# Kernel tuning notes

Measured on AMD Instinct MI355X. Metric: run time of the kernel, lower is better.

## Reference

```python
import jax, jax.numpy as jnp
import numpy as np

B, NF, H = 1024, 64, 512


def setup_inputs() -> dict:
    key = jax.random.key(0)
    ks = jax.random.split(key, 12)
    sc_in2 = 1.0 / np.sqrt(2 * H)
    sc_in1 = 1.0 / np.sqrt(H)
    inp = {
        "field_vectors": jax.random.normal(ks[0], (B, NF, H), dtype=jnp.float32),
        # and_fusion: Linear(2H->H), ReLU, Linear(H->H)
        "and_W1": jax.random.uniform(ks[1], (2 * H, H), jnp.float32, -sc_in2, sc_in2),
        "and_b1": jax.random.uniform(ks[2], (H,), jnp.float32, -sc_in2, sc_in2),
        "and_W2": jax.random.uniform(ks[3], (H, H), jnp.float32, -sc_in1, sc_in1),
        "and_b2": jax.random.uniform(ks[4], (H,), jnp.float32, -sc_in1, sc_in1),
        # or_fusion: Linear(2H->H), ReLU, Linear(H->H)
        "or_W1": jax.random.uniform(ks[5], (2 * H, H), jnp.float32, -sc_in2, sc_in2),
        "or_b1": jax.random.uniform(ks[6], (H,), jnp.float32, -sc_in2, sc_in2),
        "or_W2": jax.random.uniform(ks[7], (H, H), jnp.float32, -sc_in1, sc_in1),
        "or_b2": jax.random.uniform(ks[8], (H,), jnp.float32, -sc_in1, sc_in1),
        # not_transform: Linear(H->H), Tanh
        "not_W": jax.random.uniform(ks[9], (H, H), jnp.float32, -sc_in1, sc_in1),
        "not_b": jax.random.uniform(ks[10], (H,), jnp.float32, -sc_in1, sc_in1),
        # Disjoint index structure so the torch skip-set logic is a no-op:
        # 'and' pairs use fields 0..31, 'or' pairs use 32..47, leftovers 48..63.
        "not_idx": 48 + jnp.arange(8, dtype=jnp.int32),
        "and_pairs": jnp.arange(32, dtype=jnp.int32).reshape(16, 2),
        "or_pairs": (32 + jnp.arange(16, dtype=jnp.int32)).reshape(8, 2),
        "leftover_idx": 48 + jnp.arange(16, dtype=jnp.int32),
    }
    return inp


def _mlp2(x, W1, b1, W2, b2):
    # Linear -> ReLU -> Linear
    return jax.nn.relu(x @ W1 + b1) @ W2 + b2


def reference(field_vectors, and_W1, and_b1, and_W2, and_b2,
              or_W1, or_b1, or_W2, or_b2, not_W, not_b,
              not_idx, and_pairs, or_pairs, leftover_idx):
    # In-place 'not' transform on selected fields (Tanh(Linear))
    fv = field_vectors.at[:, not_idx].set(
        jnp.tanh(field_vectors[:, not_idx] @ not_W + not_b))
    # Gather (i, j) pairs, concat along feature dim -> [B, P, 2H]
    cat_and = jnp.concatenate([fv[:, and_pairs[:, 0]], fv[:, and_pairs[:, 1]]], axis=-1)
    fused_and = _mlp2(cat_and, and_W1, and_b1, and_W2, and_b2)  # [B, 16, H]
    cat_or = jnp.concatenate([fv[:, or_pairs[:, 0]], fv[:, or_pairs[:, 1]]], axis=-1)
    fused_or = _mlp2(cat_or, or_W1, or_b1, or_W2, or_b2)  # [B, 8, H]
    # Stack order matches torch loop: and results, or results, untouched fields
    return jnp.concatenate([fused_and, fused_or, fv[:, leftover_idx]], axis=1)
```

## Files before the change

### kernel.cpp

```cpp
#include <hip/hip_runtime.h>
#include <hip/hip_bf16.h>
#include <math.h>

typedef __attribute__((ext_vector_type(8))) __bf16 bf16x8;
typedef __attribute__((ext_vector_type(4))) float f32x4;

__device__ __forceinline__ unsigned short f2bf(float f) {
    union { float f; unsigned u; } v; v.f = f;
    unsigned r = v.u + 0x7fffu + ((v.u >> 16) & 1u);
    return (unsigned short)(r >> 16);
}
__device__ __forceinline__ unsigned int pk(float a, float b) {
    union { float f; unsigned u; } x, y; x.f = a; y.f = b;
    unsigned ra = (x.u + 0x7fffu + ((x.u >> 16) & 1u)) >> 16;
    unsigned rb = (y.u + 0x7fffu + ((y.u >> 16) & 1u)) & 0xffff0000u;
    return ra | rb;
}

__device__ __forceinline__ void gl2lds16(const unsigned short* g, unsigned short* l) {
    __builtin_amdgcn_global_load_lds(
        (const __attribute__((address_space(1))) unsigned int*)(g),
        (__attribute__((address_space(3))) unsigned int*)(l), 16, 0, 0);
}

struct SetupArgs {
    const int *and_pairs, *or_pairs, *not_idx, *lidx;
    int* tbl;
    const float* W[5];
    unsigned short* WT[5];
    int K[5], N[5];
    int tstart[6];
};

__global__ __launch_bounds__(256) void setup_kernel(SetupArgs a) {
    __shared__ float tile[64][65];
    const int blk = blockIdx.x;
    const int tid = threadIdx.x;

    if (blk == 0) {
        if (tid < 64) {
            const int f = tid;
            int u = 0;
            for (int i = 0; i < 32; i++) u |= (a.and_pairs[i] == f);
            for (int i = 0; i < 16; i++) u |= (a.or_pairs[i] == f);
            int isnot = 0;
            for (int i = 0; i < 8; i++)  isnot |= (a.not_idx[i] == f);
            int ls = -1;
            for (int l = 0; l < 16; l++) if (a.lidx[l] == f) ls = l;
            if (isnot) ls = -1;
            a.tbl[f] = (u | isnot) | ((ls + 1) << 8);
        }
        return;
    }

    const int bx = blk - 1;
    int m = 0;
    while (bx >= a.tstart[m + 1]) m++;
    const float* src = a.W[m];
    unsigned short* dst = a.WT[m];
    const int K = a.K[m], N = a.N[m];
    const int t = bx - a.tstart[m];
    const int ntn = N >> 6;
    const int tk = t / ntn, tn = t % ntn;
    const int c = tid & 63, r0 = tid >> 6;
    #pragma unroll
    for (int r = r0; r < 64; r += 4)
        tile[r][c] = src[(size_t)(tk * 64 + r) * N + tn * 64 + c];
    __syncthreads();
    const int l = tid & 63;
    #pragma unroll
    for (int fi = tid >> 6; fi < 8; fi += 4) {
        const int ktl = fi & 1, cgl = fi >> 1;
        const int kt = tk * 2 + ktl, cg = tn * 4 + cgl;
        const int kb = ktl * 32 + (l >> 4) * 8;
        const int nb = cgl * 16 + (l & 15);
        uint4 o;
        o.x = pk(tile[kb + 0][nb], tile[kb + 1][nb]);
        o.y = pk(tile[kb + 2][nb], tile[kb + 3][nb]);
        o.z = pk(tile[kb + 4][nb], tile[kb + 5][nb]);
        o.w = pk(tile[kb + 6][nb], tile[kb + 7][nb]);
        ((uint4*)dst)[((size_t)kt * 32 + cg) * 64 + l] = o;
    }
}

struct PrepArgs {
    const float* fv;
    unsigned short* fvb;
    const int* tbl;
    float* out;
};

__global__ __launch_bounds__(256) void prep_kernel(PrepArgs a) {
    const int t = blockIdx.x * 256 + threadIdx.x;
    const size_t e = (size_t)t * 8;
    const int c = (int)(e & 511);
    const int f = (int)((e >> 9) & 63);
    const int b = (int)(e >> 15);
    const float4 v0 = *(const float4*)(a.fv + e);
    const float4 v1 = *(const float4*)(a.fv + e + 4);
    const int tb = a.tbl[f];
    const int u  = tb & 0xff;
    const int ls = (tb >> 8) - 1;
    if (u) {
        uint4 o;
        o.x = pk(v0.x, v0.y); o.y = pk(v0.z, v0.w);
        o.z = pk(v1.x, v1.y); o.w = pk(v1.z, v1.w);
        ((uint4*)a.fvb)[t] = o;
    }
    if (ls >= 0) {
        float* d = a.out + ((size_t)b * 40 + 24 + ls) * 512 + c;
        *(float4*)(d)     = v0;
        *(float4*)(d + 4) = v1;
    }
}

#define LOADB(DST, WTP, KD, K0)                                              \
    _Pragma("unroll") for (int ni = 0; ni < 8; ni++)                         \
        DST[ni] = *(const bf16x8*)((WTP) +                                   \
            ((((size_t)(K0) >> 5) * 32 + cg0 + ni) << 9) + (lane << 3));

#define MMAC(BF, AF)                                                         \
    _Pragma("unroll") for (int mi = 0; mi < 4; mi++)                         \
    _Pragma("unroll") for (int ni = 0; ni < 8; ni++)                         \
        acc[mi][ni] = __builtin_amdgcn_mfma_f32_16x16x32_bf16(               \
            AF[mi], BF[ni], acc[mi][ni], 0, 0, 0);

#define L1BAR()                                                              \
    asm volatile("s_waitcnt vmcnt(9) lgkmcnt(0)" ::: "memory");              \
    asm volatile("s_barrier" ::: "memory");

template <int P, int K1, int SRCM, int PATH, int QBASE>
__device__ __forceinline__ void fused_seg(
    const unsigned short* __restrict__ A,
    const int* __restrict__ idx,
    const unsigned short* __restrict__ W1T,
    const float* __restrict__ b1,
    const unsigned short* __restrict__ W2T,
    const float* __restrict__ b2,
    float* __restrict__ out,
    const int* __restrict__ leftover,
    int local,
    unsigned short* As, unsigned short* hid) {

    const int tid  = threadIdx.x;
    const int lane = tid & 63, w = tid >> 6;
    const int ln15 = lane & 15;
    const int kq   = lane >> 4;
    const int wn   = w * 128;
    const int cg0  = w * 8;
    const int m0   = local * 64;

    const int skin = ((lane & 3) ^ ((lane >> 2) & 3)) * 8;
    const unsigned short *ar0, *ar1;
    {
        const int m = m0 + w * 16 + (lane >> 2);
        if constexpr (SRCM == 0) {
            const int b = m / P, p = m % P;
            ar0 = A + ((size_t)b * 64 + idx[2 * p]) * 512;
            ar1 = A + ((size_t)b * 64 + idx[2 * p + 1]) * 512;
        } else {
            const int b = m >> 3, i = m & 7;
            ar0 = A + ((size_t)b * 64 + idx[i]) * 512;
            ar1 = ar0;
        }
    }
    auto stageA = [&](int buf, int t) {
        const int k0 = t * 32;
        const unsigned short* src;
        if constexpr (SRCM == 0)
            src = (k0 >= 512 ? ar1 + (k0 - 512) : ar0 + k0) + skin;
        else
            src = ar0 + k0 + skin;
        gl2lds16(src, &As[buf * 2048 + w * 512]);
    };
    const int xsel = (kq ^ (lane & 3)) * 8;

    f32x4 acc[4][8];
    #pragma unroll
    for (int mi = 0; mi < 4; mi++)
        #pragma unroll
        for (int ni = 0; ni < 8; ni++)
            acc[mi][ni] = f32x4{0.f, 0.f, 0.f, 0.f};

    bf16x8 bA[8], bB[8];

    constexpr int NT1 = K1 / 32;
    stageA(0, 0);
    stageA(1, 1);
    __builtin_amdgcn_sched_barrier(0);
    LOADB(bA, W1T, K1, 0);

    for (int h = 0; h < NT1; h += 2) {
        L1BAR();
        if (h + 2 < NT1) stageA((h + 2) & 3, h + 2);
        __builtin_amdgcn_sched_barrier(0);
        LOADB(bB, W1T, K1, (h + 1) * 32);
        bf16x8 af[4];
        #pragma unroll
        for (int mi = 0; mi < 4; mi++)
            af[mi] = *(const bf16x8*)&As[(h & 3) * 2048 +
                                         (mi * 16 + ln15) * 32 + xsel];
        MMAC(bA, af);
        __builtin_amdgcn_sched_barrier(0);
        L1BAR();
        if (h + 3 < NT1) stageA((h + 3) & 3, h + 3);
        __builtin_amdgcn_sched_barrier(0);
        if (h + 2 < NT1) { LOADB(bA, W1T, K1, (h + 2) * 32); }
        #pragma unroll
        for (int mi = 0; mi < 4; mi++)
            af[mi] = *(const bf16x8*)&As[((h + 1) & 3) * 2048 +
                                         (mi * 16 + ln15) * 32 + xsel];
        MMAC(bB, af);
        __builtin_amdgcn_sched_barrier(0);
    }

    if constexpr (PATH == 2) {
        int qmap[8];
        #pragma unroll
        for (int i = 0; i < 8; i++) {
            const int f = idx[i];
            int q = 24;
            for (int l = 0; l < 16; l++)
                if (leftover[l] == f) q = 24 + l;
            qmap[i] = q;
        }
        #pragma unroll
        for (int ni = 0; ni < 8; ni++) {
            const int n = wn + ni * 16 + ln15;
            const float bv = b1[n];
            #pragma unroll
            for (int mi = 0; mi < 4; mi++)
                #pragma unroll
                for (int j = 0; j < 4; j++) {
                    const int r = mi * 16 + kq * 4 + j;
                    const int m = m0 + r;
                    const int b = m >> 3, i = m & 7;
                    out[((size_t)b * 40 + qmap[i]) * 512 + n] =
                        tanhf(acc[mi][ni][j] + bv);
                }
        }
        return;
    }

    #pragma unroll
    for (int ni = 0; ni < 8; ni++) {
        const int n  = wn + ni * 16 + ln15;
        const float bv = b1[n];
        const int c8 = n >> 3;
        const int cl = (n & 7) * 2;
        #pragma unroll
        for (int mi = 0; mi < 4; mi++)
            #pragma unroll
            for (int j = 0; j < 4; j++) {
                const int r = mi * 16 + kq * 4 + j;
                float v = acc[mi][ni][j] + bv;
                v = v > 0.f ? v : 0.f;
                *(unsigned short*)((char*)hid + r * 1024 +
                                   ((c8 ^ (r & 7)) * 16) + cl) = f2bf(v);
            }
    }
    #pragma unroll
    for (int mi = 0; mi < 4; mi++)
        #pragma unroll
        for (int ni = 0; ni < 8; ni++)
            acc[mi][ni] = f32x4{0.f, 0.f, 0.f, 0.f};
    LOADB(bA, W2T, 512, 0);
    __syncthreads();

    for (int t2 = 0; t2 < 16; t2 += 2) {
        bf16x8 af[4];
        #pragma unroll
        for (int mi = 0; mi < 4; mi++) {
            const int r = mi * 16 + ln15;
            const int c8 = t2 * 4 + kq;
            af[mi] = *(const bf16x8*)((char*)hid + r * 1024 +
                                      ((c8 ^ (r & 7)) * 16));
        }
        LOADB(bB, W2T, 512, (t2 + 1) * 32);
        MMAC(bA, af);
        #pragma unroll
        for (int mi = 0; mi < 4; mi++) {
            const int r = mi * 16 + ln15;
            const int c8 = (t2 + 1) * 4 + kq;
            af[mi] = *(const bf16x8*)((char*)hid + r * 1024 +
                                      ((c8 ^ (r & 7)) * 16));
        }
        if (t2 + 2 < 16) { LOADB(bA, W2T, 512, (t2 + 2) * 32); }
        MMAC(bB, af);
    }

    #pragma unroll
    for (int ni = 0; ni < 8; ni++) {
        const int n  = wn + ni * 16 + ln15;
        const float bv = b2[n];
        #pragma unroll
        for (int mi = 0; mi < 4; mi++)
            #pragma unroll
            for (int j = 0; j < 4; j++) {
                const int r = mi * 16 + kq * 4 + j;
                const int m = m0 + r;
                const int b = m / P, p = m % P;
                out[((size_t)b * 40 + QBASE + p) * 512 + n] =
                    acc[mi][ni][j] + bv;
            }
    }
}

struct FArgs {
    const unsigned short *fvb, *and_W1T, *and_W2T, *or_W1T, *or_W2T, *not_WT;
    const int *and_pairs, *or_pairs, *not_idx, *leftover;
    const float *and_b1, *and_b2, *or_b1, *or_b2, *not_b;
    float* out;
};

__global__ __launch_bounds__(256, 2) void fused_phase(FArgs a) {
    __shared__ __align__(16) unsigned short As[4 * 64 * 32];
    __shared__ __align__(16) unsigned short hid[64 * 512];
    const int blk = blockIdx.x;
    if (blk < 256)
        fused_seg<16, 1024, 0, 0, 0>(a.fvb, a.and_pairs, a.and_W1T, a.and_b1,
                                     a.and_W2T, a.and_b2, a.out, nullptr,
                                     blk, As, hid);
    else if (blk < 384)
        fused_seg<8, 1024, 0, 0, 16>(a.fvb, a.or_pairs, a.or_W1T, a.or_b1,
                                     a.or_W2T, a.or_b2, a.out, nullptr,
                                     blk - 256, As, hid);
    else
        fused_seg<8, 512, 1, 2, 24>(a.fvb, a.not_idx, a.not_WT, a.not_b,
                                    nullptr, nullptr, a.out, a.leftover,
                                    blk - 384, As, hid);
}

extern "C" void kernel_launch(void* const* d_in, const int* in_sizes, int n_in,
                              void* d_out, int out_size, void* d_ws, size_t ws_size,
                              hipStream_t stream) {
    const float* fv       = (const float*)d_in[0];
    const float* and_W1   = (const float*)d_in[1];
    const float* and_b1   = (const float*)d_in[2];
    const float* and_W2   = (const float*)d_in[3];
    const float* and_b2   = (const float*)d_in[4];
    const float* or_W1    = (const float*)d_in[5];
    const float* or_b1    = (const float*)d_in[6];
    const float* or_W2    = (const float*)d_in[7];
    const float* or_b2    = (const float*)d_in[8];
    const float* not_W    = (const float*)d_in[9];
    const float* not_b    = (const float*)d_in[10];
    const int* not_idx    = (const int*)d_in[11];
    const int* and_pairs  = (const int*)d_in[12];
    const int* or_pairs   = (const int*)d_in[13];
    const int* leftover   = (const int*)d_in[14];
    float* out = (float*)d_out;
    char* ws = (char*)d_ws;

    unsigned short* fvb     = (unsigned short*)(ws);
    unsigned short* and_W1T = (unsigned short*)(ws + 67108864);
    unsigned short* or_W1T  = (unsigned short*)(ws + 68157440);
    unsigned short* and_W2T = (unsigned short*)(ws + 69206016);
    unsigned short* or_W2T  = (unsigned short*)(ws + 69730304);
    unsigned short* not_WT  = (unsigned short*)(ws + 70254592);
    int*            tbl     = (int*)(ws + 70778880);

    SetupArgs sa;
    sa.and_pairs = and_pairs; sa.or_pairs = or_pairs;
    sa.not_idx = not_idx; sa.lidx = leftover; sa.tbl = tbl;
    sa.W[0] = and_W1; sa.WT[0] = and_W1T; sa.K[0] = 1024; sa.N[0] = 512;
    sa.W[1] = or_W1;  sa.WT[1] = or_W1T;  sa.K[1] = 1024; sa.N[1] = 512;
    sa.W[2] = and_W2; sa.WT[2] = and_W2T; sa.K[2] = 512;  sa.N[2] = 512;
    sa.W[3] = or_W2;  sa.WT[3] = or_W2T;  sa.K[3] = 512;  sa.N[3] = 512;
    sa.W[4] = not_W;  sa.WT[4] = not_WT;  sa.K[4] = 512;  sa.N[4] = 512;
    sa.tstart[0] = 0;   sa.tstart[1] = 128; sa.tstart[2] = 256;
    sa.tstart[3] = 320; sa.tstart[4] = 384; sa.tstart[5] = 448;
    setup_kernel<<<dim3(449), dim3(256), 0, stream>>>(sa);

    PrepArgs pa;
    pa.fv = fv; pa.fvb = fvb; pa.tbl = tbl; pa.out = out;
    prep_kernel<<<dim3(16384), dim3(256), 0, stream>>>(pa);

    FArgs fa;
    fa.fvb = fvb;
    fa.and_W1T = and_W1T; fa.and_W2T = and_W2T;
    fa.or_W1T = or_W1T;   fa.or_W2T = or_W2T;   fa.not_WT = not_WT;
    fa.and_pairs = and_pairs; fa.or_pairs = or_pairs; fa.not_idx = not_idx;
    fa.leftover = leftover;
    fa.and_b1 = and_b1; fa.and_b2 = and_b2;
    fa.or_b1 = or_b1;   fa.or_b2 = or_b2;   fa.not_b = not_b;
    fa.out = out;
    fused_phase<<<dim3(512), dim3(256), 0, stream>>>(fa);
}
```

Baseline: 312.2 us.

## Merge setup into prep kernel and split fused GEMM across eight waves

Folds the weight transpose/bf16 packing and the field-membership table into one prep kernel, computing membership per wave with ballots instead of a lookup table, so one launch is removed. The fused GEMM block grows from 256 to 512 threads, with each wave covering 64 output columns instead of 128. This halves per-wave accumulator and B-fragment registers to raise occupancy. The explicit double-buffered B-register pipeline is dropped in favour of single-step loads, so more load latency may be exposed. Only the first four waves stage A into LDS.

```diff
diff --git a/kernel.cpp b/kernel.cpp
--- a/kernel.cpp
+++ b/kernel.cpp
@@ -23,111 +23,92 @@
         (__attribute__((address_space(3))) unsigned int*)(l), 16, 0, 0);
 }
 
-struct SetupArgs {
+struct PrepArgs {
+    const float* fv;
+    unsigned short* fvb;
     const int *and_pairs, *or_pairs, *not_idx, *lidx;
-    int* tbl;
+    float* out;
     const float* W[5];
     unsigned short* WT[5];
-    int K[5], N[5];
+    int N[5];
     int tstart[6];
 };
 
-__global__ __launch_bounds__(256) void setup_kernel(SetupArgs a) {
+__global__ __launch_bounds__(256) void prep_kernel(PrepArgs a) {
     __shared__ float tile[64][65];
     const int blk = blockIdx.x;
     const int tid = threadIdx.x;
 
-    if (blk == 0) {
-        if (tid < 64) {
-            const int f = tid;
-            int u = 0;
-            for (int i = 0; i < 32; i++) u |= (a.and_pairs[i] == f);
-            for (int i = 0; i < 16; i++) u |= (a.or_pairs[i] == f);
-            int isnot = 0;
-            for (int i = 0; i < 8; i++)  isnot |= (a.not_idx[i] == f);
-            int ls = -1;
-            for (int l = 0; l < 16; l++) if (a.lidx[l] == f) ls = l;
-            if (isnot) ls = -1;
-            a.tbl[f] = (u | isnot) | ((ls + 1) << 8);
+    if (blk < 448) {
+        int m = 0;
+        while (blk >= a.tstart[m + 1]) m++;
+        const float* src = a.W[m];
+        unsigned short* dst = a.WT[m];
+        const int N = a.N[m];
+        const int t = blk - a.tstart[m];
+        const int ntn = N >> 6;
+        const int tk = t / ntn, tn = t % ntn;
+        const int c = tid & 63, r0 = tid >> 6;
+        #pragma unroll
+        for (int r = r0; r < 64; r += 4)
+            tile[r][c] = src[(size_t)(tk * 64 + r) * N + tn * 64 + c];
+        __syncthreads();
+        const int l = tid & 63;
+        #pragma unroll
+        for (int fi = tid >> 6; fi < 8; fi += 4) {
+            const int ktl = fi & 1, cgl = fi >> 1;
+            const int kt = tk * 2 + ktl, cg = tn * 4 + cgl;
+            const int kb = ktl * 32 + (l >> 4) * 8;
+            const int nb = cgl * 16 + (l & 15);
+            uint4 o;
+            o.x = pk(tile[kb + 0][nb], tile[kb + 1][nb]);
+            o.y = pk(tile[kb + 2][nb], tile[kb + 3][nb]);
+            o.z = pk(tile[kb + 4][nb], tile[kb + 5][nb]);
+            o.w = pk(tile[kb + 6][nb], tile[kb + 7][nb]);
+            ((uint4*)dst)[((size_t)kt * 32 + cg) * 64 + l] = o;
         }
         return;
     }
 
-    const int bx = blk - 1;
-    int m = 0;
-    while (bx >= a.tstart[m + 1]) m++;
-    const float* src = a.W[m];
-    unsigned short* dst = a.WT[m];
-    const int K = a.K[m], N = a.N[m];
-    const int t = bx - a.tstart[m];
-    const int ntn = N >> 6;
-    const int tk = t / ntn, tn = t % ntn;
-    const int c = tid & 63, r0 = tid >> 6;
-    #pragma unroll
-    for (int r = r0; r < 64; r += 4)
-        tile[r][c] = src[(size_t)(tk * 64 + r) * N + tn * 64 + c];
-    __syncthreads();
-    const int l = tid & 63;
-    #pragma unroll
-    for (int fi = tid >> 6; fi < 8; fi += 4) {
-        const int ktl = fi & 1, cgl = fi >> 1;
-        const int kt = tk * 2 + ktl, cg = tn * 4 + cgl;
-        const int kb = ktl * 32 + (l >> 4) * 8;
-        const int nb = cgl * 16 + (l & 15);
-        uint4 o;
-        o.x = pk(tile[kb + 0][nb], tile[kb + 1][nb]);
-        o.y = pk(tile[kb + 2][nb], tile[kb + 3][nb]);
-        o.z = pk(tile[kb + 4][nb], tile[kb + 5][nb]);
-        o.w = pk(tile[kb + 6][nb], tile[kb + 7][nb]);
-        ((uint4*)dst)[((size_t)kt * 32 + cg) * 64 + l] = o;
-    }
-}
-
-struct PrepArgs {
-    const float* fv;
-    unsigned short* fvb;
-    const int* tbl;
-    float* out;
-};
-
-__global__ __launch_bounds__(256) void prep_kernel(PrepArgs a) {
-    const int t = blockIdx.x * 256 + threadIdx.x;
+    const int t = (blk - 448) * 256 + tid;
+    const int lane = tid & 63;
     const size_t e = (size_t)t * 8;
     const int c = (int)(e & 511);
     const int f = (int)((e >> 9) & 63);
     const int b = (int)(e >> 15);
     const float4 v0 = *(const float4*)(a.fv + e);
     const float4 v1 = *(const float4*)(a.fv + e + 4);
-    const int tb = a.tbl[f];
-    const int u  = tb & 0xff;
-    const int ls = (tb >> 8) - 1;
-    if (u) {
+    const int am = (lane < 32) ? a.and_pairs[lane] : -1;
+    const int om = (lane < 16) ? a.or_pairs[lane]  : -1;
+    const int nm = (lane <  8) ? a.not_idx[lane]   : -1;
+    const int lm = (lane < 16) ? a.lidx[lane]      : -1;
+    const unsigned long long bn = __ballot(nm == f);
+    const unsigned long long bu = __ballot(am == f) | __ballot(om == f) | bn;
+    const unsigned long long bl = __ballot(lm == f);
+    if (bu) {
         uint4 o;
         o.x = pk(v0.x, v0.y); o.y = pk(v0.z, v0.w);
         o.z = pk(v1.x, v1.y); o.w = pk(v1.z, v1.w);
         ((uint4*)a.fvb)[t] = o;
     }
-    if (ls >= 0) {
+    if (bl && !bn) {
+        const int ls = (int)__builtin_ctzll(bl);
         float* d = a.out + ((size_t)b * 40 + 24 + ls) * 512 + c;
         *(float4*)(d)     = v0;
         *(float4*)(d + 4) = v1;
     }
 }
 
-#define LOADB(DST, WTP, KD, K0)                                              \
-    _Pragma("unroll") for (int ni = 0; ni < 8; ni++)                         \
+#define LOADB(DST, WTP, K0)                                                  \
+    _Pragma("unroll") for (int ni = 0; ni < 4; ni++)                         \
         DST[ni] = *(const bf16x8*)((WTP) +                                   \
             ((((size_t)(K0) >> 5) * 32 + cg0 + ni) << 9) + (lane << 3));
 
 #define MMAC(BF, AF)                                                         \
     _Pragma("unroll") for (int mi = 0; mi < 4; mi++)                         \
-    _Pragma("unroll") for (int ni = 0; ni < 8; ni++)                         \
+    _Pragma("unroll") for (int ni = 0; ni < 4; ni++)                         \
         acc[mi][ni] = __builtin_amdgcn_mfma_f32_16x16x32_bf16(               \
             AF[mi], BF[ni], acc[mi][ni], 0, 0, 0);
-
-#define L1BAR()                                                              \
-    asm volatile("s_waitcnt vmcnt(9) lgkmcnt(0)" ::: "memory");              \
-    asm volatile("s_barrier" ::: "memory");
 
 template <int P, int K1, int SRCM, int PATH, int QBASE>
 __device__ __forceinline__ void fused_seg(
@@ -146,14 +127,14 @@
     const int lane = tid & 63, w = tid >> 6;
     const int ln15 = lane & 15;
     const int kq   = lane >> 4;
-    const int wn   = w * 128;
-    const int cg0  = w * 8;
+    const int wn   = w * 64;
+    const int cg0  = w * 4;
     const int m0   = local * 64;
 
     const int skin = ((lane & 3) ^ ((lane >> 2) & 3)) * 8;
     const unsigned short *ar0, *ar1;
     {
-        const int m = m0 + w * 16 + (lane >> 2);
+        const int m = m0 + (w & 3) * 16 + (lane >> 2);
         if constexpr (SRCM == 0) {
             const int b = m / P, p = m % P;
             ar0 = A + ((size_t)b * 64 + idx[2 * p]) * 512;
@@ -171,46 +152,36 @@
             src = (k0 >= 512 ? ar1 + (k0 - 512) : ar0 + k0) + skin;
         else
             src = ar0 + k0 + skin;
-        gl2lds16(src, &As[buf * 2048 + w * 512]);
+        gl2lds16(src, &As[buf * 2048 + (w & 3) * 512]);
     };
     const int xsel = (kq ^ (lane & 3)) * 8;
 
-    f32x4 acc[4][8];
+    f32x4 acc[4][4];
     #pragma unroll
     for (int mi = 0; mi < 4; mi++)
         #pragma unroll
-        for (int ni = 0; ni < 8; ni++)
+        for (int ni = 0; ni < 4; ni++)
             acc[mi][ni] = f32x4{0.f, 0.f, 0.f, 0.f};
 
-    bf16x8 bA[8], bB[8];
+    bf16x8 bA[4];
 
     constexpr int NT1 = K1 / 32;
-    stageA(0, 0);
-    stageA(1, 1);
+    if (w < 4) { stageA(0, 0); stageA(1, 1); }
     __builtin_amdgcn_sched_barrier(0);
-    LOADB(bA, W1T, K1, 0);
-
-    for (int h = 0; h < NT1; h += 2) {
-        L1BAR();
-        if (h + 2 < NT1) stageA((h + 2) & 3, h + 2);
+
+    for (int h = 0; h < NT1; h++) {
+        asm volatile("s_waitcnt vmcnt(1) lgkmcnt(0)" ::: "memory");
+        asm volatile("s_barrier" ::: "memory");
+        LOADB(bA, W1T, h * 32);
         __builtin_amdgcn_sched_barrier(0);
-        LOADB(bB, W1T, K1, (h + 1) * 32);
+        if (w < 4 && h + 2 < NT1) stageA((h + 2) & 3, h + 2);
+        __builtin_amdgcn_sched_barrier(0);
         bf16x8 af[4];
         #pragma unroll
         for (int mi = 0; mi < 4; mi++)
             af[mi] = *(const bf16x8*)&As[(h & 3) * 2048 +
                                          (mi * 16 + ln15) * 32 + xsel];
         MMAC(bA, af);
-        __builtin_amdgcn_sched_barrier(0);
-        L1BAR();
-        if (h + 3 < NT1) stageA((h + 3) & 3, h + 3);
-        __builtin_amdgcn_sched_barrier(0);
-        if (h + 2 < NT1) { LOADB(bA, W1T, K1, (h + 2) * 32); }
-        #pragma unroll
-        for (int mi = 0; mi < 4; mi++)
-            af[mi] = *(const bf16x8*)&As[((h + 1) & 3) * 2048 +
-                                         (mi * 16 + ln15) * 32 + xsel];
-        MMAC(bB, af);
         __builtin_amdgcn_sched_barrier(0);
     }
 
@@ -225,7 +196,7 @@
             qmap[i] = q;
         }
         #pragma unroll
-        for (int ni = 0; ni < 8; ni++) {
+        for (int ni = 0; ni < 4; ni++) {
             const int n = wn + ni * 16 + ln15;
             const float bv = b1[n];
             #pragma unroll
@@ -243,7 +214,7 @@
     }
 
     #pragma unroll
-    for (int ni = 0; ni < 8; ni++) {
+    for (int ni = 0; ni < 4; ni++) {
         const int n  = wn + ni * 16 + ln15;
         const float bv = b1[n];
         const int c8 = n >> 3;
@@ -262,12 +233,12 @@
     #pragma unroll
     for (int mi = 0; mi < 4; mi++)
         #pragma unroll
-        for (int ni = 0; ni < 8; ni++)
+        for (int ni = 0; ni < 4; ni++)
             acc[mi][ni] = f32x4{0.f, 0.f, 0.f, 0.f};
-    LOADB(bA, W2T, 512, 0);
     __syncthreads();
 
-    for (int t2 = 0; t2 < 16; t2 += 2) {
+    for (int t2 = 0; t2 < 16; t2++) {
+        LOADB(bA, W2T, t2 * 32);
         bf16x8 af[4];
         #pragma unroll
         for (int mi = 0; mi < 4; mi++) {
@@ -276,21 +247,11 @@
             af[mi] = *(const bf16x8*)((char*)hid + r * 1024 +
                                       ((c8 ^ (r & 7)) * 16));
         }
-        LOADB(bB, W2T, 512, (t2 + 1) * 32);
         MMAC(bA, af);
-        #pragma unroll
-        for (int mi = 0; mi < 4; mi++) {
-            const int r = mi * 16 + ln15;
-            const int c8 = (t2 + 1) * 4 + kq;
-            af[mi] = *(const bf16x8*)((char*)hid + r * 1024 +
-                                      ((c8 ^ (r & 7)) * 16));
-        }
-        if (t2 + 2 < 16) { LOADB(bA, W2T, 512, (t2 + 2) * 32); }
-        MMAC(bB, af);
     }
 
     #pragma unroll
-    for (int ni = 0; ni < 8; ni++) {
+    for (int ni = 0; ni < 4; ni++) {
         const int n  = wn + ni * 16 + ln15;
         const float bv = b2[n];
         #pragma unroll
@@ -313,7 +274,7 @@
     float* out;
 };
 
-__global__ __launch_bounds__(256, 2) void fused_phase(FArgs a) {
+__global__ __launch_bounds__(512, 4) void fused_phase(FArgs a) {
     __shared__ __align__(16) unsigned short As[4 * 64 * 32];
     __shared__ __align__(16) unsigned short hid[64 * 512];
     const int blk = blockIdx.x;
@@ -358,23 +319,19 @@
     unsigned short* and_W2T = (unsigned short*)(ws + 69206016);
     unsigned short* or_W2T  = (unsigned short*)(ws + 69730304);
     unsigned short* not_WT  = (unsigned short*)(ws + 70254592);
-    int*            tbl     = (int*)(ws + 70778880);
-
-    SetupArgs sa;
-    sa.and_pairs = and_pairs; sa.or_pairs = or_pairs;
-    sa.not_idx = not_idx; sa.lidx = leftover; sa.tbl = tbl;
-    sa.W[0] = and_W1; sa.WT[0] = and_W1T; sa.K[0] = 1024; sa.N[0] = 512;
-    sa.W[1] = or_W1;  sa.WT[1] = or_W1T;  sa.K[1] = 1024; sa.N[1] = 512;
-    sa.W[2] = and_W2; sa.WT[2] = and_W2T; sa.K[2] = 512;  sa.N[2] = 512;
-    sa.W[3] = or_W2;  sa.WT[3] = or_W2T;  sa.K[3] = 512;  sa.N[3] = 512;
-    sa.W[4] = not_W;  sa.WT[4] = not_WT;  sa.K[4] = 512;  sa.N[4] = 512;
-    sa.tstart[0] = 0;   sa.tstart[1] = 128; sa.tstart[2] = 256;
-    sa.tstart[3] = 320; sa.tstart[4] = 384; sa.tstart[5] = 448;
-    setup_kernel<<<dim3(449), dim3(256), 0, stream>>>(sa);
 
     PrepArgs pa;
-    pa.fv = fv; pa.fvb = fvb; pa.tbl = tbl; pa.out = out;
-    prep_kernel<<<dim3(16384), dim3(256), 0, stream>>>(pa);
+    pa.fv = fv; pa.fvb = fvb; pa.out = out;
+    pa.and_pairs = and_pairs; pa.or_pairs = or_pairs;
+    pa.not_idx = not_idx; pa.lidx = leftover;
+    pa.W[0] = and_W1; pa.WT[0] = and_W1T; pa.N[0] = 512;
+    pa.W[1] = or_W1;  pa.WT[1] = or_W1T;  pa.N[1] = 512;
+    pa.W[2] = and_W2; pa.WT[2] = and_W2T; pa.N[2] = 512;
+    pa.W[3] = or_W2;  pa.WT[3] = or_W2T;  pa.N[3] = 512;
+    pa.W[4] = not_W;  pa.WT[4] = not_WT;  pa.N[4] = 512;
+    pa.tstart[0] = 0;   pa.tstart[1] = 128; pa.tstart[2] = 256;
+    pa.tstart[3] = 320; pa.tstart[4] = 384; pa.tstart[5] = 448;
+    prep_kernel<<<dim3(448 + 16384), dim3(256), 0, stream>>>(pa);
 
     FArgs fa;
     fa.fvb = fvb;
@@ -385,5 +342,5 @@
     fa.and_b1 = and_b1; fa.and_b2 = and_b2;
     fa.or_b1 = or_b1;   fa.or_b2 = or_b2;   fa.not_b = not_b;
     fa.out = out;
-    fused_phase<<<dim3(512), dim3(256), 0, stream>>>(fa);
-}
+    fused_phase<<<dim3(512), dim3(512), 0, stream>>>(fa);
+}
```

Result: faster. 302.9 us (-3.0%).
